# Kernel tuning notes

Measured on AMD Instinct MI355X. Metric: run time of the kernel, lower is better.

Reference implementation:

```python
import jax, jax.numpy as jnp
import numpy as np

D = 1024
H = 16
HD = D // H
EPS = 1e-6


def rms_norm(x, w):
    # x: [..., hd]; compute in float32 like the torch module
    xf = x.astype(jnp.float32)
    rms = jnp.sqrt(jnp.mean(xf * xf, axis=-1, keepdims=True) + EPS)
    return (xf / rms * w.astype(jnp.float32)).astype(x.dtype)


def setup_inputs() -> dict:
    key = jax.random.key(0)
    ks = jax.random.split(key, 6)
    B, S = 2, 2048
    x = jax.random.normal(ks[0], (B, S, D), dtype=jnp.float32)
    Wqkv = jax.random.normal(ks[1], (3 * D, D), dtype=jnp.float32) * (1.0 / np.sqrt(D))
    bqkv = jax.random.normal(ks[2], (3 * D,), dtype=jnp.float32) * 0.02
    Wproj = jax.random.normal(ks[3], (D, D), dtype=jnp.float32) * (1.0 / np.sqrt(D))
    bproj = jax.random.normal(ks[4], (D,), dtype=jnp.float32) * 0.02
    qn_w = jnp.ones((HD,), dtype=jnp.float32)
    kn_w = jnp.ones((HD,), dtype=jnp.float32)
    return {"x": x, "Wqkv": Wqkv, "bqkv": bqkv, "Wproj": Wproj, "bproj": bproj,
            "qn_w": qn_w, "kn_w": kn_w}


def reference(x, Wqkv, bqkv, Wproj, bproj, qn_w, kn_w):
    B, S, _ = x.shape
    # QKV projection: torch Linear is x @ W.T + b
    qkv = x @ Wqkv.T + bqkv                     # [B, S, 3D]
    qkv = qkv.reshape(B, S, 3, H, HD)
    q, k, v = qkv[:, :, 0], qkv[:, :, 1], qkv[:, :, 2]   # each [B, S, H, hd]
    q = rms_norm(q, qn_w)
    k = rms_norm(k, kn_w)
    # move heads forward: [B, H, S, hd]
    q = q.transpose(0, 2, 1, 3)
    k = k.transpose(0, 2, 1, 3)
    v = v.transpose(0, 2, 1, 3)
    scale = 1.0 / np.sqrt(HD)
    scores = jnp.einsum('bhsd,bhtd->bhst', q, k) * scale   # [B, H, S, S] (math backend)
    attn = jax.nn.softmax(scores, axis=-1)
    out = jnp.einsum('bhst,bhtd->bhsd', attn, v)            # [B, H, S, hd]
    out = out.transpose(0, 2, 1, 3).reshape(B, S, D)
    return out @ Wproj.T + bproj
```

## Files before the change

kernel.cpp:

```cpp
#include <hip/hip_runtime.h>
#include <hip/hip_bf16.h>
#include <math.h>

#define D_MODEL 1024
#define NH 16
#define HD 64
#define SEQ 2048
#define BATCH 2
#define NTOK (BATCH*SEQ)

typedef short bf16x8 __attribute__((ext_vector_type(8)));
typedef short s4 __attribute__((ext_vector_type(4)));
typedef float f32x4 __attribute__((ext_vector_type(4)));
typedef unsigned short us4 __attribute__((ext_vector_type(4)));

#define MFMA(a,b,c) __builtin_amdgcn_mfma_f32_16x16x32_bf16(a,b,c,0,0,0)

union bfu { __hip_bfloat16 b; unsigned short u; };
__device__ __forceinline__ unsigned short f2b(float f){ bfu t; t.b = __float2bfloat16(f); return t.u; }
__device__ __forceinline__ float b2f(unsigned short u){ bfu t; t.u = u; return __bfloat162float(t.b); }
__device__ __forceinline__ unsigned short f2bf(float f){
    unsigned int u = __float_as_uint(f);
    u += 0x7FFFu + ((u >> 16) & 1u);
    return (unsigned short)(u >> 16);
}

__device__ __forceinline__ void g2l16(const unsigned short* g, unsigned short* l){
    __builtin_amdgcn_global_load_lds(
        (const __attribute__((address_space(1))) unsigned int*)g,
        (__attribute__((address_space(3))) unsigned int*)l, 16, 0, 0);
}

#define OFF_X   128L
#define OFF_WQ  (OFF_X  + 4194304L)
#define OFF_BQ  (OFF_WQ + 3145728L)
#define OFF_WP  (OFF_BQ + 3072L)
#define OFF_BP  (OFF_WP + 1048576L)
#define OFF_QN  (OFF_BP + 1024L)
#define OFF_KN  (OFF_QN + 64L)
#define OFF_Q   (OFF_KN + 64L)
#define OFF_K   (OFF_Q  + 4194304L)
#define OFF_V   (OFF_K  + 4194304L)
#define OFF_A   (OFF_V  + 4194304L)


__global__ __launch_bounds__(256) void detect_kernel(
    const unsigned int* __restrict__ xraw, int* __restrict__ cnt)
{
    int i = blockIdx.x*256 + threadIdx.x;
    uint4 v = ((const uint4*)xraw)[i];
    unsigned int w[4] = {v.x, v.y, v.z, v.w};
    int local = 0;
    #pragma unroll
    for (int j=0;j<4;j++){
        local += ((w[j] & 0x7F80u) >= 0x4800u);
        local += (((w[j]>>16) & 0x7F80u) >= 0x4800u);
    }
    if (local) atomicAdd(cnt, local);
}

__global__ __launch_bounds__(256) void convert_kernel(
    const void* __restrict__ x,  const void* __restrict__ wq,
    const void* __restrict__ bq, const void* __restrict__ wp,
    const void* __restrict__ bp, const void* __restrict__ qn,
    const void* __restrict__ kn, unsigned short* __restrict__ ws,
    const int* __restrict__ cntp)
{
    const int flag = (*cntp > 256);
    long i = (long)blockIdx.x*blockDim.x + threadIdx.x;
    const long stride = (long)gridDim.x*blockDim.x;
    const long NCH = 2098208L;
    for (; i < NCH; i += stride){
        long j = i; const void* src; long off;
        if (j < 1048576L)                  { src = x;  off = OFF_X;  }
        else if ((j -= 1048576L) < 786432L){ src = wq; off = OFF_WQ; }
        else if ((j -= 786432L)  < 768L)   { src = bq; off = OFF_BQ; }
        else if ((j -= 768L)     < 262144L){ src = wp; off = OFF_WP; }
        else if ((j -= 262144L)  < 256L)   { src = bp; off = OFF_BP; }
        else if ((j -= 256L)     < 16L)    { src = qn; off = OFF_QN; }
        else      { j -= 16L;                src = kn; off = OFF_KN; }
        us4 o;
        if (flag){
            float4 v = ((const float4*)src)[j];
            o.x = f2b(v.x); o.y = f2b(v.y); o.z = f2b(v.z); o.w = f2b(v.w);
        } else {
            o = ((const us4*)src)[j];
        }
        *(us4*)(ws + off + j*4) = o;
    }
}

__global__ __launch_bounds__(256) void qkv_kernel(
    const unsigned short* __restrict__ x,
    const unsigned short* __restrict__ Wqkv,
    const unsigned short* __restrict__ bqkv,
    const unsigned short* __restrict__ qn_w,
    const unsigned short* __restrict__ kn_w,
    unsigned short* __restrict__ qbuf,
    unsigned short* __restrict__ kbuf,
    unsigned short* __restrict__ vbuf)
{
    __shared__ __align__(16) unsigned short tA[128*32];
    __shared__ __align__(16) unsigned short tB[128*32];
    const int tid  = threadIdx.x;
    const int w    = tid >> 6, lane = tid & 63, quad = lane >> 4, c = lane & 15;
    const int m0 = blockIdx.y*128, n0 = blockIdx.x*128;
    const int am = (w>>1)*64, bn = (w&1)*64;

    f32x4 acc[4][4];
    for (int mi=0;mi<4;mi++) for (int ni=0;ni<4;ni++) acc[mi][ni] = {0.f,0.f,0.f,0.f};

    const int i0 = tid, i1 = tid + 256;
    const long ga0 = (long)(m0 + (i0>>2))*D_MODEL + (i0&3)*8;
    const long ga1 = (long)(m0 + (i1>>2))*D_MODEL + (i1&3)*8;
    const long gb0 = (long)(n0 + (i0>>2))*D_MODEL + (i0&3)*8;
    const long gb1 = (long)(n0 + (i1>>2))*D_MODEL + (i1&3)*8;

    for (int k0=0;k0<D_MODEL;k0+=32){
        g2l16(x    + ga0 + k0, tA + i0*8);
        g2l16(x    + ga1 + k0, tA + i1*8);
        g2l16(Wqkv + gb0 + k0, tB + i0*8);
        g2l16(Wqkv + gb1 + k0, tB + i1*8);
        __syncthreads();
        bf16x8 a[4], b[4];
        for (int mi=0;mi<4;mi++) a[mi] = *(const bf16x8*)(tA + (am + mi*16 + c)*32 + quad*8);
        for (int ni=0;ni<4;ni++) b[ni] = *(const bf16x8*)(tB + (bn + ni*16 + c)*32 + quad*8);
        for (int mi=0;mi<4;mi++)
            for (int ni=0;ni<4;ni++)
                acc[mi][ni] = MFMA(a[mi], b[ni], acc[mi][ni]);
        __syncthreads();
    }

    const int nw = n0 + bn, mw = m0 + am;
    const int region = nw >> 10;
    const int h      = (nw & 1023) >> 6;
    float bias[4], wn[4];
    for (int ni=0;ni<4;ni++){
        bias[ni] = b2f(bqkv[nw + ni*16 + c]);
        wn[ni]   = 1.0f;
    }
    if (region==0) for (int ni=0;ni<4;ni++) wn[ni] = b2f(qn_w[ni*16+c]) * 0.18033688f;
    if (region==1) for (int ni=0;ni<4;ni++) wn[ni] = b2f(kn_w[ni*16+c]);

    for (int mi=0;mi<4;mi++){
        for (int ni=0;ni<4;ni++)
            for (int r=0;r<4;r++) acc[mi][ni][r] += bias[ni];

        float scale_r[4];
        if (region < 2){
            for (int r=0;r<4;r++){
                float ss = 0.f;
                for (int ni=0;ni<4;ni++){ float v2 = acc[mi][ni][r]; ss += v2*v2; }
                ss += __shfl_xor(ss, 1, 64);
                ss += __shfl_xor(ss, 2, 64);
                ss += __shfl_xor(ss, 4, 64);
                ss += __shfl_xor(ss, 8, 64);
                scale_r[r] = rsqrtf(ss*(1.0f/64.0f) + 1e-6f);
            }
        } else {
            for (int r=0;r<4;r++) scale_r[r] = 1.0f;
        }

        for (int r=0;r<4;r++){
            int m = mw + mi*16 + quad*4 + r;
            int bidx = m >> 11, s = m & 2047;
            long bb = (long)(bidx*NH + h)*SEQ*HD;
            if (region == 0){
                long base = bb + (long)s*HD;
                for (int ni=0;ni<4;ni++)
                    qbuf[base + ni*16 + c] = f2bf(acc[mi][ni][r] * scale_r[r] * wn[ni]);
            } else if (region == 1){
                long tb = bb + (long)(s>>6)*4096;
                for (int ni=0;ni<4;ni++){
                    int d = ni*16 + c;
                    long idx = tb + (long)((s&63)*8 + ((d>>3) ^ (s&7)))*8 + (d&7);
                    kbuf[idx] = f2bf(acc[mi][ni][r] * scale_r[r] * wn[ni]);
                }
            } else {
                long tb = bb + (long)(s>>6)*4096;
                int ch2  = (s>>4)&3;
                int fb   = ((s>>2)&3)*4;
                int mloc = s&3;
                for (int ni=0;ni<4;ni++){
                    int d = ni*16 + c;
                    int f = fb + (((d>>1) + ch2)&3);
                    long idx = tb + (long)d*64 + f*4 + mloc;
                    vbuf[idx] = f2bf(acc[mi][ni][r]);
                }
            }
        }
    }
}

__global__ __launch_bounds__(256, 4) void attn_kernel(
    const unsigned short* __restrict__ qbuf,
    const unsigned short* __restrict__ kts,
    const unsigned short* __restrict__ vts,
    unsigned short* __restrict__ abuf)
{
    const int tid = threadIdx.x, w = tid>>6, lane = tid&63, quad = lane>>4, c = lane&15;
    const int bh = blockIdx.y, qt = blockIdx.x;
    const unsigned short* qb = qbuf + (long)bh*SEQ*HD;
    const unsigned short* kb = kts + (long)bh*SEQ*HD;
    const unsigned short* vb = vts + (long)bh*SEQ*HD;
    const int qbase = qt*64 + w*16;
    const int cq = c & 7;

    __shared__ __align__(16) unsigned short KT[2][4096];
    __shared__ __align__(16) unsigned short VT[2][4096];

    bf16x8 aq[2];
    #pragma unroll
    for (int ks=0;ks<2;ks++)
        aq[ks] = *(const bf16x8*)(qb + (long)(qbase + c)*HD + ks*32 + quad*8);

    f32x4 o[4];
    #pragma unroll
    for (int nt=0;nt<4;nt++) o[nt] = {0.f,0.f,0.f,0.f};
    f32x4 l4 = {0.f,0.f,0.f,0.f};

    auto stage = [&](const unsigned short* src, unsigned short* dst){
        g2l16(src + tid*8,        dst + tid*8);
        g2l16(src + 2048 + tid*8, dst + 2048 + tid*8);
    };

    stage(kb, KT[0]); stage(vb, VT[0]);
    __syncthreads();

    for (int kt2=0; kt2<SEQ/64; kt2++){
        const unsigned short* ktl = KT[kt2&1];
        const unsigned short* vtl = VT[kt2&1];
        if (kt2 < SEQ/64 - 1){
            stage(kb + (kt2+1)*4096, KT[(kt2&1)^1]);
            stage(vb + (kt2+1)*4096, VT[(kt2&1)^1]);
        }

        bf16x8 kf[4][2];
        #pragma unroll
        for (int mt=0;mt<4;mt++)
            #pragma unroll
            for (int ks=0;ks<2;ks++)
                kf[mt][ks] = *(const bf16x8*)(ktl + ((mt*16+c)*8 + ((ks*4+quad)^cq))*8);

        f32x4 z4[4];
        #pragma unroll
        for (int mt=0;mt<4;mt++){
            f32x4 t = {0.f,0.f,0.f,0.f};
            t = MFMA(kf[mt][0], aq[0], t);
            t = MFMA(kf[mt][1], aq[1], t);
            z4[mt] = t;
        }

        unsigned int pk[4][2];
        #pragma unroll
        for (int mt=0;mt<4;mt++){
            float p0 = __builtin_amdgcn_exp2f(z4[mt][0]);
            float p1 = __builtin_amdgcn_exp2f(z4[mt][1]);
            float p2 = __builtin_amdgcn_exp2f(z4[mt][2]);
            float p3 = __builtin_amdgcn_exp2f(z4[mt][3]);
            l4[0] += p0; l4[1] += p1; l4[2] += p2; l4[3] += p3;
            pk[mt][0] = __builtin_amdgcn_perm(__float_as_uint(p1), __float_as_uint(p0), 0x07060302u);
            pk[mt][1] = __builtin_amdgcn_perm(__float_as_uint(p3), __float_as_uint(p2), 0x07060302u);
        }

        #pragma unroll
        for (int ks=0;ks<2;ks++){
            union { unsigned int u[4]; bf16x8 v; } pB;
            pB.u[0] = pk[2*ks][0];   pB.u[1] = pk[2*ks][1];
            pB.u[2] = pk[2*ks+1][0]; pB.u[3] = pk[2*ks+1][1];
            #pragma unroll
            for (int nt=0;nt<4;nt++){
                const int dv = nt*16 + c;
                const unsigned short* vbase = vtl + dv*64;
                int flo = quad*4 + (((dv>>1) + ks*2    )&3);
                int fhi = quad*4 + (((dv>>1) + ks*2 + 1)&3);
                uint2 lo = *(const uint2*)(vbase + flo*4);
                uint2 hi = *(const uint2*)(vbase + fhi*4);
                union { unsigned int u[4]; bf16x8 v; } vv;
                vv.u[0]=lo.x; vv.u[1]=lo.y; vv.u[2]=hi.x; vv.u[3]=hi.y;
                o[nt] = MFMA(vv.v, pB.v, o[nt]);
            }
        }
        __syncthreads();
    }

    float l_loc = (l4[0]+l4[1]) + (l4[2]+l4[3]);
    l_loc += __shfl_xor(l_loc, 16, 64);
    l_loc += __shfl_xor(l_loc, 32, 64);
    float inv = 1.0f / l_loc;

    const int b = bh >> 4, h = bh & 15;
    long base = ((long)(b*SEQ + qbase + c)*NH + h)*HD;
    #pragma unroll
    for (int nt=0;nt<4;nt++){
        us4 pkd;
        #pragma unroll
        for (int r=0;r<4;r++) pkd[r] = f2bf(o[nt][r]*inv);
        *(us4*)(abuf + base + nt*16 + quad*4) = pkd;
    }
}

__global__ __launch_bounds__(256) void proj_kernel(
    const unsigned short* __restrict__ abuf,
    const unsigned short* __restrict__ Wp,
    const unsigned short* __restrict__ bp,
    void* __restrict__ outv,
    const int* __restrict__ cntp)
{
    __shared__ __align__(16) unsigned short tA[128*32];
    __shared__ __align__(16) unsigned short tB[64*32];
    const int tid  = threadIdx.x;
    const int w    = tid >> 6, lane = tid & 63, quad = lane >> 4, c = lane & 15;
    const int m0 = blockIdx.y*128, n0 = blockIdx.x*64;
    const int am = (w>>1)*64, bn = (w&1)*32;
    const int flag = (*cntp > 256);

    f32x4 acc[4][2];
    for (int mi=0;mi<4;mi++) for (int ni=0;ni<2;ni++) acc[mi][ni] = {0.f,0.f,0.f,0.f};

    const int i0 = tid, i1 = tid + 256;
    const long ga0 = (long)(m0 + (i0>>2))*D_MODEL + (i0&3)*8;
    const long ga1 = (long)(m0 + (i1>>2))*D_MODEL + (i1&3)*8;
    const long gb0 = (long)(n0 + (i0>>2))*D_MODEL + (i0&3)*8;

    for (int k0=0;k0<D_MODEL;k0+=32){
        g2l16(abuf + ga0 + k0, tA + i0*8);
        g2l16(abuf + ga1 + k0, tA + i1*8);
        g2l16(Wp   + gb0 + k0, tB + i0*8);
        __syncthreads();
        bf16x8 a[4], b[2];
        for (int mi=0;mi<4;mi++) a[mi] = *(const bf16x8*)(tA + (am + mi*16 + c)*32 + quad*8);
        for (int ni=0;ni<2;ni++) b[ni] = *(const bf16x8*)(tB + (bn + ni*16 + c)*32 + quad*8);
        for (int mi=0;mi<4;mi++)
            for (int ni=0;ni<2;ni++)
                acc[mi][ni] = MFMA(a[mi], b[ni], acc[mi][ni]);
        __syncthreads();
    }

    float bias[2];
    for (int ni=0;ni<2;ni++) bias[ni] = b2f(bp[n0 + bn + ni*16 + c]);

    for (int mi=0;mi<4;mi++)
        for (int r=0;r<4;r++){
            long m = m0 + am + mi*16 + quad*4 + r;
            for (int ni=0;ni<2;ni++){
                float val = acc[mi][ni][r] + bias[ni];
                long idx = m*D_MODEL + n0 + bn + ni*16 + c;
                if (flag) ((float*)outv)[idx] = val;
                else      ((unsigned short*)outv)[idx] = f2bf(val);
            }
        }
}

extern "C" void kernel_launch(void* const* d_in, const int* in_sizes, int n_in,
                              void* d_out, int out_size, void* d_ws, size_t ws_size,
                              hipStream_t stream)
{
    unsigned short* ws = (unsigned short*)d_ws;
    int* cnt = (int*)d_ws;

    hipMemsetAsync(cnt, 0, 4, stream);
    hipLaunchKernelGGL(detect_kernel, dim3(16), dim3(256), 0, stream,
                       (const unsigned int*)d_in[0], cnt);
    hipLaunchKernelGGL(convert_kernel, dim3(2048), dim3(256), 0, stream,
                       d_in[0], d_in[1], d_in[2], d_in[3], d_in[4], d_in[5], d_in[6],
                       ws, cnt);
    hipLaunchKernelGGL(qkv_kernel,  dim3(24,32), dim3(256), 0, stream,
                       ws+OFF_X, ws+OFF_WQ, ws+OFF_BQ, ws+OFF_QN, ws+OFF_KN,
                       ws+OFF_Q, ws+OFF_K, ws+OFF_V);
    hipLaunchKernelGGL(attn_kernel, dim3(32,32), dim3(256), 0, stream,
                       ws+OFF_Q, ws+OFF_K, ws+OFF_V, ws+OFF_A);
    hipLaunchKernelGGL(proj_kernel, dim3(16,32), dim3(256), 0, stream,
                       ws+OFF_A, ws+OFF_WP, ws+OFF_BP, d_out, cnt);
}
```

Before: 223.1 us.

## Widen GEMM K-tile to 64 with XOR-swizzled LDS layout in QKV and proj

Both GEMM kernels (QKV projection and output projection) now stage 64-wide K slices in shared memory instead of 32, which halves the number of barrier pairs per K loop. Global-to-LDS loads place 16-byte chunks using an XOR swizzle (chunk ^ row&7), and the fragment reads apply the same swizzle, to avoid LDS bank conflicts on the wider rows. The QKV kernel also gets a launch-bounds occupancy hint of 3 blocks. The trade is doubled LDS per block, which may reduce occupancy.

```diff
diff --git a/kernel.cpp b/kernel.cpp
--- a/kernel.cpp
+++ b/kernel.cpp
@@ -90,7 +90,7 @@
     }
 }
 
-__global__ __launch_bounds__(256) void qkv_kernel(
+__global__ __launch_bounds__(256, 3) void qkv_kernel(
     const unsigned short* __restrict__ x,
     const unsigned short* __restrict__ Wqkv,
     const unsigned short* __restrict__ bqkv,
@@ -100,34 +100,53 @@
     unsigned short* __restrict__ kbuf,
     unsigned short* __restrict__ vbuf)
 {
-    __shared__ __align__(16) unsigned short tA[128*32];
-    __shared__ __align__(16) unsigned short tB[128*32];
+    __shared__ __align__(16) unsigned short tA[128*64];
+    __shared__ __align__(16) unsigned short tB[128*64];
     const int tid  = threadIdx.x;
     const int w    = tid >> 6, lane = tid & 63, quad = lane >> 4, c = lane & 15;
     const int m0 = blockIdx.y*128, n0 = blockIdx.x*128;
     const int am = (w>>1)*64, bn = (w&1)*64;
+    const int cx = c & 7;
 
     f32x4 acc[4][4];
     for (int mi=0;mi<4;mi++) for (int ni=0;ni<4;ni++) acc[mi][ni] = {0.f,0.f,0.f,0.f};
 
-    const int i0 = tid, i1 = tid + 256;
-    const long ga0 = (long)(m0 + (i0>>2))*D_MODEL + (i0&3)*8;
-    const long ga1 = (long)(m0 + (i1>>2))*D_MODEL + (i1&3)*8;
-    const long gb0 = (long)(n0 + (i0>>2))*D_MODEL + (i0&3)*8;
-    const long gb1 = (long)(n0 + (i1>>2))*D_MODEL + (i1&3)*8;
-
-    for (int k0=0;k0<D_MODEL;k0+=32){
-        g2l16(x    + ga0 + k0, tA + i0*8);
-        g2l16(x    + ga1 + k0, tA + i1*8);
-        g2l16(Wqkv + gb0 + k0, tB + i0*8);
-        g2l16(Wqkv + gb1 + k0, tB + i1*8);
+    long gaL[4], gbL[4];
+    #pragma unroll
+    for (int L=0;L<4;L++){
+        int i = L*256 + tid;
+        int r = i>>3, cc = (i&7) ^ (r&7);
+        gaL[L] = (long)(m0 + r)*D_MODEL + cc*8;
+        gbL[L] = (long)(n0 + r)*D_MODEL + cc*8;
+    }
+
+    for (int k0=0;k0<D_MODEL;k0+=64){
+        #pragma unroll
+        for (int L=0;L<4;L++){
+            g2l16(x    + gaL[L] + k0, tA + (L*256+tid)*8);
+            g2l16(Wqkv + gbL[L] + k0, tB + (L*256+tid)*8);
+        }
         __syncthreads();
-        bf16x8 a[4], b[4];
-        for (int mi=0;mi<4;mi++) a[mi] = *(const bf16x8*)(tA + (am + mi*16 + c)*32 + quad*8);
-        for (int ni=0;ni<4;ni++) b[ni] = *(const bf16x8*)(tB + (bn + ni*16 + c)*32 + quad*8);
-        for (int mi=0;mi<4;mi++)
-            for (int ni=0;ni<4;ni++)
-                acc[mi][ni] = MFMA(a[mi], b[ni], acc[mi][ni]);
+        #pragma unroll
+        for (int ks=0;ks<2;ks++){
+            const int kq = (ks*4 + quad) ^ cx;
+            bf16x8 a[4], b[4];
+            #pragma unroll
+            for (int mi=0;mi<4;mi++){
+                int row = am + mi*16 + c;
+                a[mi] = *(const bf16x8*)(tA + (row*8 + kq)*8);
+            }
+            #pragma unroll
+            for (int ni=0;ni<4;ni++){
+                int row = bn + ni*16 + c;
+                b[ni] = *(const bf16x8*)(tB + (row*8 + kq)*8);
+            }
+            #pragma unroll
+            for (int mi=0;mi<4;mi++)
+                #pragma unroll
+                for (int ni=0;ni<4;ni++)
+                    acc[mi][ni] = MFMA(a[mi], b[ni], acc[mi][ni]);
+        }
         __syncthreads();
     }
 
@@ -307,33 +326,60 @@
     void* __restrict__ outv,
     const int* __restrict__ cntp)
 {
-    __shared__ __align__(16) unsigned short tA[128*32];
-    __shared__ __align__(16) unsigned short tB[64*32];
+    __shared__ __align__(16) unsigned short tA[128*64];
+    __shared__ __align__(16) unsigned short tB[64*64];
     const int tid  = threadIdx.x;
     const int w    = tid >> 6, lane = tid & 63, quad = lane >> 4, c = lane & 15;
     const int m0 = blockIdx.y*128, n0 = blockIdx.x*64;
     const int am = (w>>1)*64, bn = (w&1)*32;
+    const int cx = c & 7;
     const int flag = (*cntp > 256);
 
     f32x4 acc[4][2];
     for (int mi=0;mi<4;mi++) for (int ni=0;ni<2;ni++) acc[mi][ni] = {0.f,0.f,0.f,0.f};
 
-    const int i0 = tid, i1 = tid + 256;
-    const long ga0 = (long)(m0 + (i0>>2))*D_MODEL + (i0&3)*8;
-    const long ga1 = (long)(m0 + (i1>>2))*D_MODEL + (i1&3)*8;
-    const long gb0 = (long)(n0 + (i0>>2))*D_MODEL + (i0&3)*8;
-
-    for (int k0=0;k0<D_MODEL;k0+=32){
-        g2l16(abuf + ga0 + k0, tA + i0*8);
-        g2l16(abuf + ga1 + k0, tA + i1*8);
-        g2l16(Wp   + gb0 + k0, tB + i0*8);
+    long gaL[4], gbL[2];
+    #pragma unroll
+    for (int L=0;L<4;L++){
+        int i = L*256 + tid;
+        int r = i>>3, cc = (i&7) ^ (r&7);
+        gaL[L] = (long)(m0 + r)*D_MODEL + cc*8;
+    }
+    #pragma unroll
+    for (int L=0;L<2;L++){
+        int i = L*256 + tid;
+        int r = i>>3, cc = (i&7) ^ (r&7);
+        gbL[L] = (long)(n0 + r)*D_MODEL + cc*8;
+    }
+
+    for (int k0=0;k0<D_MODEL;k0+=64){
+        #pragma unroll
+        for (int L=0;L<4;L++)
+            g2l16(abuf + gaL[L] + k0, tA + (L*256+tid)*8);
+        #pragma unroll
+        for (int L=0;L<2;L++)
+            g2l16(Wp + gbL[L] + k0, tB + (L*256+tid)*8);
         __syncthreads();
-        bf16x8 a[4], b[2];
-        for (int mi=0;mi<4;mi++) a[mi] = *(const bf16x8*)(tA + (am + mi*16 + c)*32 + quad*8);
-        for (int ni=0;ni<2;ni++) b[ni] = *(const bf16x8*)(tB + (bn + ni*16 + c)*32 + quad*8);
-        for (int mi=0;mi<4;mi++)
-            for (int ni=0;ni<2;ni++)
-                acc[mi][ni] = MFMA(a[mi], b[ni], acc[mi][ni]);
+        #pragma unroll
+        for (int ks=0;ks<2;ks++){
+            const int kq = (ks*4 + quad) ^ cx;
+            bf16x8 a[4], b[2];
+            #pragma unroll
+            for (int mi=0;mi<4;mi++){
+                int row = am + mi*16 + c;
+                a[mi] = *(const bf16x8*)(tA + (row*8 + kq)*8);
+            }
+            #pragma unroll
+            for (int ni=0;ni<2;ni++){
+                int row = bn + ni*16 + c;
+                b[ni] = *(const bf16x8*)(tB + (row*8 + kq)*8);
+            }
+            #pragma unroll
+            for (int mi=0;mi<4;mi++)
+                #pragma unroll
+                for (int ni=0;ni<2;ni++)
+                    acc[mi][ni] = MFMA(a[mi], b[ni], acc[mi][ni]);
+        }
         __syncthreads();
     }
 
```

Measured after the change: 411.1 us. 1.84x slower.

## Double-buffer LDS tiles and XOR-swizzle layout in QKV and projection GEMMs

Applied to the files above, without the earlier changes.

Both GEMM kernels now use two LDS buffers, so the next K-tile is loaded while the current one feeds the MFMAs, which removes one barrier per iteration. The shared-memory layout is XOR-swizzled on the 16-byte chunk index, applied to the global source offset on load and to the read offset on compute, to reduce LDS bank conflicts. Inner loops are explicitly unrolled. LDS use per block doubles, which may lower occupancy. The attention kernel, which is likely the dominant cost, is unchanged.

```diff
diff --git a/kernel.cpp b/kernel.cpp
--- a/kernel.cpp
+++ b/kernel.cpp
@@ -100,32 +100,53 @@
     unsigned short* __restrict__ kbuf,
     unsigned short* __restrict__ vbuf)
 {
-    __shared__ __align__(16) unsigned short tA[128*32];
-    __shared__ __align__(16) unsigned short tB[128*32];
+    __shared__ __align__(16) unsigned short tA[2][128*32];
+    __shared__ __align__(16) unsigned short tB[2][128*32];
     const int tid  = threadIdx.x;
     const int w    = tid >> 6, lane = tid & 63, quad = lane >> 4, c = lane & 15;
     const int m0 = blockIdx.y*128, n0 = blockIdx.x*128;
     const int am = (w>>1)*64, bn = (w&1)*64;
+    const int kq = quad ^ ((c>>1)&3);
 
     f32x4 acc[4][4];
     for (int mi=0;mi<4;mi++) for (int ni=0;ni<4;ni++) acc[mi][ni] = {0.f,0.f,0.f,0.f};
 
     const int i0 = tid, i1 = tid + 256;
-    const long ga0 = (long)(m0 + (i0>>2))*D_MODEL + (i0&3)*8;
-    const long ga1 = (long)(m0 + (i1>>2))*D_MODEL + (i1&3)*8;
-    const long gb0 = (long)(n0 + (i0>>2))*D_MODEL + (i0&3)*8;
-    const long gb1 = (long)(n0 + (i1>>2))*D_MODEL + (i1&3)*8;
-
-    for (int k0=0;k0<D_MODEL;k0+=32){
-        g2l16(x    + ga0 + k0, tA + i0*8);
-        g2l16(x    + ga1 + k0, tA + i1*8);
-        g2l16(Wqkv + gb0 + k0, tB + i0*8);
-        g2l16(Wqkv + gb1 + k0, tB + i1*8);
-        __syncthreads();
+    const int r0 = i0>>2, cc0 = (i0&3) ^ ((r0>>1)&3);
+    const int r1 = i1>>2, cc1 = (i1&3) ^ ((r1>>1)&3);
+    const long gaA0 = (long)(m0 + r0)*D_MODEL + cc0*8;
+    const long gaA1 = (long)(m0 + r1)*D_MODEL + cc1*8;
+    const long gbB0 = (long)(n0 + r0)*D_MODEL + cc0*8;
+    const long gbB1 = (long)(n0 + r1)*D_MODEL + cc1*8;
+
+    g2l16(x    + gaA0, tA[0] + i0*8);
+    g2l16(x    + gaA1, tA[0] + i1*8);
+    g2l16(Wqkv + gbB0, tB[0] + i0*8);
+    g2l16(Wqkv + gbB1, tB[0] + i1*8);
+    __syncthreads();
+
+    for (int t=0; t<32; t++){
+        if (t < 31){
+            const int k1 = (t+1)*32;
+            unsigned short* dA = tA[(t&1)^1];
+            unsigned short* dB = tB[(t&1)^1];
+            g2l16(x    + gaA0 + k1, dA + i0*8);
+            g2l16(x    + gaA1 + k1, dA + i1*8);
+            g2l16(Wqkv + gbB0 + k1, dB + i0*8);
+            g2l16(Wqkv + gbB1 + k1, dB + i1*8);
+        }
+        const unsigned short* A = tA[t&1];
+        const unsigned short* B = tB[t&1];
         bf16x8 a[4], b[4];
-        for (int mi=0;mi<4;mi++) a[mi] = *(const bf16x8*)(tA + (am + mi*16 + c)*32 + quad*8);
-        for (int ni=0;ni<4;ni++) b[ni] = *(const bf16x8*)(tB + (bn + ni*16 + c)*32 + quad*8);
+        #pragma unroll
         for (int mi=0;mi<4;mi++)
+            a[mi] = *(const bf16x8*)(A + ((am + mi*16 + c)*4 + kq)*8);
+        #pragma unroll
+        for (int ni=0;ni<4;ni++)
+            b[ni] = *(const bf16x8*)(B + ((bn + ni*16 + c)*4 + kq)*8);
+        #pragma unroll
+        for (int mi=0;mi<4;mi++)
+            #pragma unroll
             for (int ni=0;ni<4;ni++)
                 acc[mi][ni] = MFMA(a[mi], b[ni], acc[mi][ni]);
         __syncthreads();
@@ -307,31 +328,51 @@
     void* __restrict__ outv,
     const int* __restrict__ cntp)
 {
-    __shared__ __align__(16) unsigned short tA[128*32];
-    __shared__ __align__(16) unsigned short tB[64*32];
+    __shared__ __align__(16) unsigned short tA[2][128*32];
+    __shared__ __align__(16) unsigned short tB[2][64*32];
     const int tid  = threadIdx.x;
     const int w    = tid >> 6, lane = tid & 63, quad = lane >> 4, c = lane & 15;
     const int m0 = blockIdx.y*128, n0 = blockIdx.x*64;
     const int am = (w>>1)*64, bn = (w&1)*32;
+    const int kq = quad ^ ((c>>1)&3);
     const int flag = (*cntp > 256);
 
     f32x4 acc[4][2];
     for (int mi=0;mi<4;mi++) for (int ni=0;ni<2;ni++) acc[mi][ni] = {0.f,0.f,0.f,0.f};
 
     const int i0 = tid, i1 = tid + 256;
-    const long ga0 = (long)(m0 + (i0>>2))*D_MODEL + (i0&3)*8;
-    const long ga1 = (long)(m0 + (i1>>2))*D_MODEL + (i1&3)*8;
-    const long gb0 = (long)(n0 + (i0>>2))*D_MODEL + (i0&3)*8;
-
-    for (int k0=0;k0<D_MODEL;k0+=32){
-        g2l16(abuf + ga0 + k0, tA + i0*8);
-        g2l16(abuf + ga1 + k0, tA + i1*8);
-        g2l16(Wp   + gb0 + k0, tB + i0*8);
-        __syncthreads();
+    const int r0 = i0>>2, cc0 = (i0&3) ^ ((r0>>1)&3);
+    const int r1 = i1>>2, cc1 = (i1&3) ^ ((r1>>1)&3);
+    const long gaA0 = (long)(m0 + r0)*D_MODEL + cc0*8;
+    const long gaA1 = (long)(m0 + r1)*D_MODEL + cc1*8;
+    const long gbB0 = (long)(n0 + r0)*D_MODEL + cc0*8;
+
+    g2l16(abuf + gaA0, tA[0] + i0*8);
+    g2l16(abuf + gaA1, tA[0] + i1*8);
+    g2l16(Wp   + gbB0, tB[0] + i0*8);
+    __syncthreads();
+
+    for (int t=0; t<32; t++){
+        if (t < 31){
+            const int k1 = (t+1)*32;
+            unsigned short* dA = tA[(t&1)^1];
+            unsigned short* dB = tB[(t&1)^1];
+            g2l16(abuf + gaA0 + k1, dA + i0*8);
+            g2l16(abuf + gaA1 + k1, dA + i1*8);
+            g2l16(Wp   + gbB0 + k1, dB + i0*8);
+        }
+        const unsigned short* A = tA[t&1];
+        const unsigned short* B = tB[t&1];
         bf16x8 a[4], b[2];
-        for (int mi=0;mi<4;mi++) a[mi] = *(const bf16x8*)(tA + (am + mi*16 + c)*32 + quad*8);
-        for (int ni=0;ni<2;ni++) b[ni] = *(const bf16x8*)(tB + (bn + ni*16 + c)*32 + quad*8);
+        #pragma unroll
         for (int mi=0;mi<4;mi++)
+            a[mi] = *(const bf16x8*)(A + ((am + mi*16 + c)*4 + kq)*8);
+        #pragma unroll
+        for (int ni=0;ni<2;ni++)
+            b[ni] = *(const bf16x8*)(B + ((bn + ni*16 + c)*4 + kq)*8);
+        #pragma unroll
+        for (int mi=0;mi<4;mi++)
+            #pragma unroll
             for (int ni=0;ni<2;ni++)
                 acc[mi][ni] = MFMA(a[mi], b[ni], acc[mi][ni]);
         __syncthreads();
```

Measured after the change: 230.3 us. 3.2% more time.

## Double-buffer QKV and proj GEMM tiles with XOR-swizzled LDS layout

Applied to the files above, without the earlier changes.

The QKV and projection GEMM kernels now use two LDS buffers per operand. The next k-tile's global-to-LDS copy is issued before computing the current tile, which halves the barriers per k-step and overlaps loads with MFMA work. The LDS chunk index is XOR-swizzled by row to reduce bank conflicts on the 16-byte fragment reads. The attention loop is manually unrolled by two with separate named buffers so buffer selection is static. This doubles LDS use per block, which may reduce occupancy.

```diff
diff --git a/kernel.cpp b/kernel.cpp
--- a/kernel.cpp
+++ b/kernel.cpp
@@ -100,36 +100,60 @@
     unsigned short* __restrict__ kbuf,
     unsigned short* __restrict__ vbuf)
 {
-    __shared__ __align__(16) unsigned short tA[128*32];
-    __shared__ __align__(16) unsigned short tB[128*32];
+    __shared__ __align__(16) unsigned short tA0[128*32];
+    __shared__ __align__(16) unsigned short tA1[128*32];
+    __shared__ __align__(16) unsigned short tB0[128*32];
+    __shared__ __align__(16) unsigned short tB1[128*32];
     const int tid  = threadIdx.x;
     const int w    = tid >> 6, lane = tid & 63, quad = lane >> 4, c = lane & 15;
     const int m0 = blockIdx.y*128, n0 = blockIdx.x*128;
     const int am = (w>>1)*64, bn = (w&1)*64;
+    const int kq = quad ^ ((c>>1)&3);
 
     f32x4 acc[4][4];
     for (int mi=0;mi<4;mi++) for (int ni=0;ni<4;ni++) acc[mi][ni] = {0.f,0.f,0.f,0.f};
 
     const int i0 = tid, i1 = tid + 256;
-    const long ga0 = (long)(m0 + (i0>>2))*D_MODEL + (i0&3)*8;
-    const long ga1 = (long)(m0 + (i1>>2))*D_MODEL + (i1&3)*8;
-    const long gb0 = (long)(n0 + (i0>>2))*D_MODEL + (i0&3)*8;
-    const long gb1 = (long)(n0 + (i1>>2))*D_MODEL + (i1&3)*8;
-
-    for (int k0=0;k0<D_MODEL;k0+=32){
-        g2l16(x    + ga0 + k0, tA + i0*8);
-        g2l16(x    + ga1 + k0, tA + i1*8);
-        g2l16(Wqkv + gb0 + k0, tB + i0*8);
-        g2l16(Wqkv + gb1 + k0, tB + i1*8);
-        __syncthreads();
-        bf16x8 a[4], b[4];
-        for (int mi=0;mi<4;mi++) a[mi] = *(const bf16x8*)(tA + (am + mi*16 + c)*32 + quad*8);
-        for (int ni=0;ni<4;ni++) b[ni] = *(const bf16x8*)(tB + (bn + ni*16 + c)*32 + quad*8);
-        for (int mi=0;mi<4;mi++)
-            for (int ni=0;ni<4;ni++)
-                acc[mi][ni] = MFMA(a[mi], b[ni], acc[mi][ni]);
-        __syncthreads();
-    }
+    const int r0 = i0>>2, cc0 = (i0&3) ^ ((r0>>1)&3);
+    const int r1 = i1>>2, cc1 = (i1&3) ^ ((r1>>1)&3);
+    const long gaA0 = (long)(m0 + r0)*D_MODEL + cc0*8;
+    const long gaA1 = (long)(m0 + r1)*D_MODEL + cc1*8;
+    const long gbB0 = (long)(n0 + r0)*D_MODEL + cc0*8;
+    const long gbB1 = (long)(n0 + r1)*D_MODEL + cc1*8;
+
+#define QKV_STAGE(BUFA, BUFB, T) do{ const int kk_ = (T)*32; \
+    g2l16(x    + gaA0 + kk_, BUFA + i0*8); \
+    g2l16(x    + gaA1 + kk_, BUFA + i1*8); \
+    g2l16(Wqkv + gbB0 + kk_, BUFB + i0*8); \
+    g2l16(Wqkv + gbB1 + kk_, BUFB + i1*8); }while(0)
+
+#define QKV_COMP(BUFA, BUFB) do{ \
+    bf16x8 a_[4], b_[4]; \
+    _Pragma("unroll") \
+    for (int mi=0;mi<4;mi++) \
+        a_[mi] = *(const bf16x8*)(BUFA + ((am + mi*16 + c)*4 + kq)*8); \
+    _Pragma("unroll") \
+    for (int ni=0;ni<4;ni++) \
+        b_[ni] = *(const bf16x8*)(BUFB + ((bn + ni*16 + c)*4 + kq)*8); \
+    _Pragma("unroll") \
+    for (int mi=0;mi<4;mi++) \
+        _Pragma("unroll") \
+        for (int ni=0;ni<4;ni++) \
+            acc[mi][ni] = MFMA(a_[mi], b_[ni], acc[mi][ni]); }while(0)
+
+    QKV_STAGE(tA0, tB0, 0);
+    __syncthreads();
+
+    for (int t=0; t<32; t+=2){
+        QKV_STAGE(tA1, tB1, t+1);
+        QKV_COMP(tA0, tB0);
+        __syncthreads();
+        if (t+2 < 32) QKV_STAGE(tA0, tB0, t+2);
+        QKV_COMP(tA1, tB1);
+        __syncthreads();
+    }
+#undef QKV_STAGE
+#undef QKV_COMP
 
     const int nw = n0 + bn, mw = m0 + am;
     const int region = nw >> 10;
@@ -206,8 +230,10 @@
     const int qbase = qt*64 + w*16;
     const int cq = c & 7;
 
-    __shared__ __align__(16) unsigned short KT[2][4096];
-    __shared__ __align__(16) unsigned short VT[2][4096];
+    __shared__ __align__(16) unsigned short KT0[4096];
+    __shared__ __align__(16) unsigned short KT1[4096];
+    __shared__ __align__(16) unsigned short VT0[4096];
+    __shared__ __align__(16) unsigned short VT1[4096];
 
     bf16x8 aq[2];
     #pragma unroll
@@ -219,70 +245,72 @@
     for (int nt=0;nt<4;nt++) o[nt] = {0.f,0.f,0.f,0.f};
     f32x4 l4 = {0.f,0.f,0.f,0.f};
 
-    auto stage = [&](const unsigned short* src, unsigned short* dst){
-        g2l16(src + tid*8,        dst + tid*8);
-        g2l16(src + 2048 + tid*8, dst + 2048 + tid*8);
-    };
-
-    stage(kb, KT[0]); stage(vb, VT[0]);
+#define STAGE2(SRC, DST) do{ \
+    g2l16((SRC) + tid*8,        DST + tid*8); \
+    g2l16((SRC) + 2048 + tid*8, DST + 2048 + tid*8); }while(0)
+
+#define ATTN_TILE(KTB, VTB) do{ \
+    bf16x8 kf_[4][2]; \
+    _Pragma("unroll") \
+    for (int mt=0;mt<4;mt++) \
+        _Pragma("unroll") \
+        for (int ks=0;ks<2;ks++) \
+            kf_[mt][ks] = *(const bf16x8*)(KTB + ((mt*16+c)*8 + ((ks*4+quad)^cq))*8); \
+    f32x4 z4_[4]; \
+    _Pragma("unroll") \
+    for (int mt=0;mt<4;mt++){ \
+        f32x4 t_ = {0.f,0.f,0.f,0.f}; \
+        t_ = MFMA(kf_[mt][0], aq[0], t_); \
+        t_ = MFMA(kf_[mt][1], aq[1], t_); \
+        z4_[mt] = t_; \
+    } \
+    unsigned int pk_[4][2]; \
+    _Pragma("unroll") \
+    for (int mt=0;mt<4;mt++){ \
+        float p0 = __builtin_amdgcn_exp2f(z4_[mt][0]); \
+        float p1 = __builtin_amdgcn_exp2f(z4_[mt][1]); \
+        float p2 = __builtin_amdgcn_exp2f(z4_[mt][2]); \
+        float p3 = __builtin_amdgcn_exp2f(z4_[mt][3]); \
+        l4[0] += p0; l4[1] += p1; l4[2] += p2; l4[3] += p3; \
+        pk_[mt][0] = __builtin_amdgcn_perm(__float_as_uint(p1), __float_as_uint(p0), 0x07060302u); \
+        pk_[mt][1] = __builtin_amdgcn_perm(__float_as_uint(p3), __float_as_uint(p2), 0x07060302u); \
+    } \
+    _Pragma("unroll") \
+    for (int ks=0;ks<2;ks++){ \
+        union { unsigned int u[4]; bf16x8 v; } pB_; \
+        pB_.u[0] = pk_[2*ks][0];   pB_.u[1] = pk_[2*ks][1]; \
+        pB_.u[2] = pk_[2*ks+1][0]; pB_.u[3] = pk_[2*ks+1][1]; \
+        _Pragma("unroll") \
+        for (int nt=0;nt<4;nt++){ \
+            const int dv_ = nt*16 + c; \
+            const unsigned short* vbase_ = VTB + dv_*64; \
+            int flo_ = quad*4 + (((dv_>>1) + ks*2    )&3); \
+            int fhi_ = quad*4 + (((dv_>>1) + ks*2 + 1)&3); \
+            uint2 lo_ = *(const uint2*)(vbase_ + flo_*4); \
+            uint2 hi_ = *(const uint2*)(vbase_ + fhi_*4); \
+            union { unsigned int u[4]; bf16x8 v; } vv_; \
+            vv_.u[0]=lo_.x; vv_.u[1]=lo_.y; vv_.u[2]=hi_.x; vv_.u[3]=hi_.y; \
+            o[nt] = MFMA(vv_.v, pB_.v, o[nt]); \
+        } \
+    } }while(0)
+
+    STAGE2(kb, KT0); STAGE2(vb, VT0);
     __syncthreads();
 
-    for (int kt2=0; kt2<SEQ/64; kt2++){
-        const unsigned short* ktl = KT[kt2&1];
-        const unsigned short* vtl = VT[kt2&1];
-        if (kt2 < SEQ/64 - 1){
-            stage(kb + (kt2+1)*4096, KT[(kt2&1)^1]);
-            stage(vb + (kt2+1)*4096, VT[(kt2&1)^1]);
+    for (int kt2=0; kt2<SEQ/64; kt2+=2){
+        STAGE2(kb + (kt2+1)*4096, KT1);
+        STAGE2(vb + (kt2+1)*4096, VT1);
+        ATTN_TILE(KT0, VT0);
+        __syncthreads();
+        if (kt2+2 < SEQ/64){
+            STAGE2(kb + (kt2+2)*4096, KT0);
+            STAGE2(vb + (kt2+2)*4096, VT0);
         }
-
-        bf16x8 kf[4][2];
-        #pragma unroll
-        for (int mt=0;mt<4;mt++)
-            #pragma unroll
-            for (int ks=0;ks<2;ks++)
-                kf[mt][ks] = *(const bf16x8*)(ktl + ((mt*16+c)*8 + ((ks*4+quad)^cq))*8);
-
-        f32x4 z4[4];
-        #pragma unroll
-        for (int mt=0;mt<4;mt++){
-            f32x4 t = {0.f,0.f,0.f,0.f};
-            t = MFMA(kf[mt][0], aq[0], t);
-            t = MFMA(kf[mt][1], aq[1], t);
-            z4[mt] = t;
-        }
-
-        unsigned int pk[4][2];
-        #pragma unroll
-        for (int mt=0;mt<4;mt++){
-            float p0 = __builtin_amdgcn_exp2f(z4[mt][0]);
-            float p1 = __builtin_amdgcn_exp2f(z4[mt][1]);
-            float p2 = __builtin_amdgcn_exp2f(z4[mt][2]);
-            float p3 = __builtin_amdgcn_exp2f(z4[mt][3]);
-            l4[0] += p0; l4[1] += p1; l4[2] += p2; l4[3] += p3;
-            pk[mt][0] = __builtin_amdgcn_perm(__float_as_uint(p1), __float_as_uint(p0), 0x07060302u);
-            pk[mt][1] = __builtin_amdgcn_perm(__float_as_uint(p3), __float_as_uint(p2), 0x07060302u);
-        }
-
-        #pragma unroll
-        for (int ks=0;ks<2;ks++){
-            union { unsigned int u[4]; bf16x8 v; } pB;
-            pB.u[0] = pk[2*ks][0];   pB.u[1] = pk[2*ks][1];
-            pB.u[2] = pk[2*ks+1][0]; pB.u[3] = pk[2*ks+1][1];
-            #pragma unroll
-            for (int nt=0;nt<4;nt++){
-                const int dv = nt*16 + c;
-                const unsigned short* vbase = vtl + dv*64;
-                int flo = quad*4 + (((dv>>1) + ks*2    )&3);
-                int fhi = quad*4 + (((dv>>1) + ks*2 + 1)&3);
-                uint2 lo = *(const uint2*)(vbase + flo*4);
-                uint2 hi = *(const uint2*)(vbase + fhi*4);
-                union { unsigned int u[4]; bf16x8 v; } vv;
-                vv.u[0]=lo.x; vv.u[1]=lo.y; vv.u[2]=hi.x; vv.u[3]=hi.y;
-                o[nt] = MFMA(vv.v, pB.v, o[nt]);
-            }
-        }
-        __syncthreads();
-    }
+        ATTN_TILE(KT1, VT1);
+        __syncthreads();
+    }
+#undef STAGE2
+#undef ATTN_TILE
 
     float l_loc = (l4[0]+l4[1]) + (l4[2]+l4[3]);
     l_loc += __shfl_xor(l_loc, 16, 64);
@@ -307,35 +335,59 @@
     void* __restrict__ outv,
     const int* __restrict__ cntp)
 {
-    __shared__ __align__(16) unsigned short tA[128*32];
-    __shared__ __align__(16) unsigned short tB[64*32];
+    __shared__ __align__(16) unsigned short tA0[128*32];
+    __shared__ __align__(16) unsigned short tA1[128*32];
+    __shared__ __align__(16) unsigned short tB0[64*32];
+    __shared__ __align__(16) unsigned short tB1[64*32];
     const int tid  = threadIdx.x;
     const int w    = tid >> 6, lane = tid & 63, quad = lane >> 4, c = lane & 15;
     const int m0 = blockIdx.y*128, n0 = blockIdx.x*64;
     const int am = (w>>1)*64, bn = (w&1)*32;
+    const int kq = quad ^ ((c>>1)&3);
     const int flag = (*cntp > 256);
 
     f32x4 acc[4][2];
     for (int mi=0;mi<4;mi++) for (int ni=0;ni<2;ni++) acc[mi][ni] = {0.f,0.f,0.f,0.f};
 
     const int i0 = tid, i1 = tid + 256;
-    const long ga0 = (long)(m0 + (i0>>2))*D_MODEL + (i0&3)*8;
-    const long ga1 = (long)(m0 + (i1>>2))*D_MODEL + (i1&3)*8;
-    const long gb0 = (long)(n0 + (i0>>2))*D_MODEL + (i0&3)*8;
-
-    for (int k0=0;k0<D_MODEL;k0+=32){
-        g2l16(abuf + ga0 + k0, tA + i0*8);
-        g2l16(abuf + ga1 + k0, tA + i1*8);
-        g2l16(Wp   + gb0 + k0, tB + i0*8);
-        __syncthreads();
-        bf16x8 a[4], b[2];
-        for (int mi=0;mi<4;mi++) a[mi] = *(const bf16x8*)(tA + (am + mi*16 + c)*32 + quad*8);
-        for (int ni=0;ni<2;ni++) b[ni] = *(const bf16x8*)(tB + (bn + ni*16 + c)*32 + quad*8);
-        for (int mi=0;mi<4;mi++)
-            for (int ni=0;ni<2;ni++)
-                acc[mi][ni] = MFMA(a[mi], b[ni], acc[mi][ni]);
-        __syncthreads();
-    }
+    const int r0 = i0>>2, cc0 = (i0&3) ^ ((r0>>1)&3);
+    const int r1 = i1>>2, cc1 = (i1&3) ^ ((r1>>1)&3);
+    const long gaA0 = (long)(m0 + r0)*D_MODEL + cc0*8;
+    const long gaA1 = (long)(m0 + r1)*D_MODEL + cc1*8;
+    const long gbB0 = (long)(n0 + r0)*D_MODEL + cc0*8;
+
+#define PROJ_STAGE(BUFA, BUFB, T) do{ const int kk_ = (T)*32; \
+    g2l16(abuf + gaA0 + kk_, BUFA + i0*8); \
+    g2l16(abuf + gaA1 + kk_, BUFA + i1*8); \
+    g2l16(Wp   + gbB0 + kk_, BUFB + i0*8); }while(0)
+
+#define PROJ_COMP(BUFA, BUFB) do{ \
+    bf16x8 a_[4], b_[2]; \
+    _Pragma("unroll") \
+    for (int mi=0;mi<4;mi++) \
+        a_[mi] = *(const bf16x8*)(BUFA + ((am + mi*16 + c)*4 + kq)*8); \
+    _Pragma("unroll") \
+    for (int ni=0;ni<2;ni++) \
+        b_[ni] = *(const bf16x8*)(BUFB + ((bn + ni*16 + c)*4 + kq)*8); \
+    _Pragma("unroll") \
+    for (int mi=0;mi<4;mi++) \
+        _Pragma("unroll") \
+        for (int ni=0;ni<2;ni++) \
+            acc[mi][ni] = MFMA(a_[mi], b_[ni], acc[mi][ni]); }while(0)
+
+    PROJ_STAGE(tA0, tB0, 0);
+    __syncthreads();
+
+    for (int t=0; t<32; t+=2){
+        PROJ_STAGE(tA1, tB1, t+1);
+        PROJ_COMP(tA0, tB0);
+        __syncthreads();
+        if (t+2 < 32) PROJ_STAGE(tA0, tB0, t+2);
+        PROJ_COMP(tA1, tB1);
+        __syncthreads();
+    }
+#undef PROJ_STAGE
+#undef PROJ_COMP
 
     float bias[2];
     for (int ni=0;ni<2;ni++) bias[ni] = b2f(bp[n0 + bn + ni*16 + c]);
```

Result: faster. 213.7 us (-4.2%).
